# Performance work log

Measured on AMD Instinct MI355X. Metric: run time of the kernel, lower is better.

## Reference

```python
import jax, jax.numpy as jnp
import numpy as np

EPS = 1e-6
BANDWIDTH = 10


def _norm_last(x):
    return x / jnp.sum(x, axis=-1, keepdims=True)


def _causal_linear_branch(Q, K, V, eps):
    # Q,K: [N,L,H,E] feature-mapped; V: [N,L,H,D]
    Q = _norm_last(Q)
    K = _norm_last(K)
    Kcum = jnp.cumsum(K, axis=1)                                   # [N,L,H,E]
    Z = 1.0 / (jnp.einsum('nlhe,nlhe->nlh', Q, Kcum) + eps)        # [N,L,H]
    # causal_dot_product: running sum of outer products K_s V_s^T
    S = jnp.cumsum(K[..., :, None] * V[..., None, :], axis=1)       # [N,L,H,E,D]
    Vn = jnp.einsum('nlhe,nlhed->nlhd', Q, S)                       # [N,L,H,D]
    return Vn * Z[..., None]


def setup_inputs() -> dict:
    key = jax.random.key(0)
    k1, k2, k3, k4 = jax.random.split(key, 4)
    N, L, H, E = 2, 2048, 8, 32
    return {
        'queries': jax.random.normal(k1, (N, L, H, E), dtype=jnp.float32),
        'keys': jax.random.normal(k2, (N, L, H, E), dtype=jnp.float32),
        'values': jax.random.normal(k3, (N, L, H, E), dtype=jnp.float32),
        'key_lengths': jnp.ones((N, L), dtype=jnp.float32),
        'W1': 0.02 * jax.random.normal(k4, (1, 1, H, E), dtype=jnp.float32),
        'W2': jnp.ones((1, 1, H, E), dtype=jnp.float32) * 0.5,
        'W3': jnp.ones((1, 1, H, E), dtype=jnp.float32) * 0.5,
    }


def reference(queries, keys, values, key_lengths, W1, W2, W3):
    klen = key_lengths[:, :, None, None]
    # kernel 1: elu feature map phi(x) = elu(x) + 1
    Q1 = jax.nn.elu(queries) + 1.0
    K1 = (jax.nn.elu(keys) + 1.0) * klen
    LV = W2 * _causal_linear_branch(Q1, K1, values, EPS)
    # kernel 2: squared elu feature map phi(x) = (elu(x) + 1)^2
    Q2 = (jax.nn.elu(queries) + 1.0) ** 2
    K2 = ((jax.nn.elu(keys) + 1.0) ** 2) * klen
    LV = LV + W3 * _causal_linear_branch(Q2, K2, values, EPS)
    # sparse near-field: banded causal softmax attention
    N, L, H, E = queries.shape
    temp = 1.0 / np.sqrt(E).astype(np.float32)
    QK = jnp.einsum('nlhe,nshe->nhls', queries * temp, keys)       # [N,H,L,S]
    li = jnp.arange(L)[:, None]
    si = jnp.arange(L)[None, :]
    band = (si <= li) & (si > li - BANDWIDTH)                      # keep band of width `bandwidth`
    QK = jnp.where(band[None, None], QK, -jnp.inf)
    A = jax.nn.softmax(QK, axis=-1)                                # dropout is identity (p=0 / eval)
    SV = jnp.einsum('nhls,nshd->nlhd', A, values)
    return W1 * SV + LV
```

## Files before the change

### kernel.cpp

```cpp
#include <hip/hip_runtime.h>
#include <cmath>

constexpr int NN = 2;
constexpr int LL = 2048;
constexpr int HH = 8;
constexpr int EE = 32;
constexpr int CC = 32;
constexpr int NCH = LL / CC;
constexpr int NB  = NN * HH * NCH;
constexpr int BWD = 10;
constexpr int REC  = 2 * (EE * EE + EE);
constexpr int R16  = REC * 2 / 16;
constexpr int OFF_S1 = 0, OFF_K1 = 1024, OFF_S2 = 1056, OFF_K2 = 2080;
constexpr int SK = EE + 4;
constexpr int SB = 40;

using f32x16 = __attribute__((ext_vector_type(16))) float;
using s16x8  = __attribute__((ext_vector_type(8)))  short;

__device__ __forceinline__ float elu1(float x) {
    return x > 0.f ? x + 1.f : __expf(x);
}
__device__ __forceinline__ unsigned short bfr(float x) {
    union { float f; unsigned u; } v; v.f = x;
    return (unsigned short)((v.u + 0x7FFFu + ((v.u >> 16) & 1u)) >> 16);
}
__device__ __forceinline__ float bf2f(unsigned short b) {
    union { unsigned u; float f; } v; v.u = ((unsigned)b) << 16;
    return v.f;
}

__global__ __launch_bounds__(256) void chunksum_kernel(
    const float* __restrict__ Kin, const float* __restrict__ Vin,
    unsigned short* __restrict__ ws)
{
    __shared__ float K1n[CC][SK];
    __shared__ float K2n[CC][SK];
    __shared__ float Vs [CC][SK];

    const int b  = blockIdx.x;
    const int c  = b & (NCH - 1);
    const int nh = b >> 6;
    const int t  = threadIdx.x;
    const int lane = t & 31;
    const int grp  = t >> 5;

    for (int r = grp; r < CC; r += 8) {
        const int l = c * CC + r;
        const int base = ((nh >> 3) * LL + l) * HH * EE + (nh & 7) * EE + lane;
        const float k = Kin[base];
        const float v = Vin[base];
        const float f1 = elu1(k);
        const float f2 = f1 * f1;
        float s1 = f1, s2 = f2;
        #pragma unroll
        for (int m = 1; m < 32; m <<= 1) {
            s1 += __shfl_xor(s1, m, 32);
            s2 += __shfl_xor(s2, m, 32);
        }
        K1n[r][lane] = f1 * __builtin_amdgcn_rcpf(s1);
        K2n[r][lane] = f2 * __builtin_amdgcn_rcpf(s2);
        Vs [r][lane] = v;
    }
    __syncthreads();

    const int d  = t >> 3;
    const int e0 = (t & 7) * 4;
    float a1x=0.f,a1y=0.f,a1z=0.f,a1w=0.f;
    float a2x=0.f,a2y=0.f,a2z=0.f,a2w=0.f;
    float k1x=0.f,k1y=0.f,k1z=0.f,k1w=0.f;
    float k2x=0.f,k2y=0.f,k2z=0.f,k2w=0.f;
    for (int j = 0; j < CC; ++j) {
        const float vv = Vs[j][d];
        const float4 k1 = *(const float4*)&K1n[j][e0];
        const float4 k2 = *(const float4*)&K2n[j][e0];
        k1x += k1.x; k1y += k1.y; k1z += k1.z; k1w += k1.w;
        k2x += k2.x; k2y += k2.y; k2z += k2.z; k2w += k2.w;
        a1x += vv * k1.x; a1y += vv * k1.y; a1z += vv * k1.z; a1w += vv * k1.w;
        a2x += vv * k2.x; a2y += vv * k2.y; a2z += vv * k2.z; a2w += vv * k2.w;
    }
    unsigned short* wb = ws + (size_t)b * REC;
    ushort4 o1 = { bfr(a1x), bfr(a1y), bfr(a1z), bfr(a1w) };
    ushort4 o2 = { bfr(a2x), bfr(a2y), bfr(a2z), bfr(a2w) };
    *(ushort4*)&wb[OFF_S1 + d * EE + e0] = o1;
    *(ushort4*)&wb[OFF_S2 + d * EE + e0] = o2;
    if (d == 0) {
        ushort4 s1v = { bfr(k1x), bfr(k1y), bfr(k1z), bfr(k1w) };
        ushort4 s2v = { bfr(k2x), bfr(k2y), bfr(k2z), bfr(k2w) };
        *(ushort4*)&wb[OFF_K1 + e0] = s1v;
        *(ushort4*)&wb[OFF_K2 + e0] = s2v;
    }
}

__global__ __launch_bounds__(192) void prefix_kernel(unsigned short* __restrict__ ws)
{
    const int g = blockIdx.x / 11;
    const int e = (blockIdx.x % 11) * 192 + threadIdx.x;
    unsigned short* base = ws + (size_t)g * NCH * REC + e;
    float run = 0.f;
    {
        unsigned short v[32];
        #pragma unroll
        for (int c = 0; c < 32; ++c) v[c] = base[(size_t)c * REC];
        #pragma unroll
        for (int c = 0; c < 32; ++c) {
            base[(size_t)c * REC] = bfr(run);
            run += bf2f(v[c]);
        }
    }
    {
        unsigned short v[32];
        #pragma unroll
        for (int c = 0; c < 32; ++c) v[c] = base[(size_t)(32 + c) * REC];
        #pragma unroll
        for (int c = 0; c < 32; ++c) {
            base[(size_t)(32 + c) * REC] = bfr(run);
            run += bf2f(v[c]);
        }
    }
}

__global__ __launch_bounds__(256) void fused_kernel(
    const float* __restrict__ Qin, const float* __restrict__ Kin,
    const float* __restrict__ Vin,
    const float* __restrict__ W1, const float* __restrict__ W2,
    const float* __restrict__ W3, const unsigned short* __restrict__ ws,
    float* __restrict__ out)
{
    __shared__ float Vs [CC + 9][SK];
    __shared__ __align__(16) unsigned short Qfb[CC][SB];
    __shared__ __align__(16) unsigned short Kfb[CC][SB];
    __shared__ __align__(16) unsigned short Pb1[CC][SB];
    __shared__ __align__(16) unsigned short Pb2[CC][SB];
    __shared__ float Ob1[CC][SK];
    __shared__ float Ob2[CC][SK];
    __shared__ __align__(16) union {
        float kr[(CC + 9) * SK];
        unsigned short sp[REC];
    } U;

    const int b  = blockIdx.x;
    const int c  = b & (NCH - 1);
    const int nh = b >> 6;
    const int h  = nh & 7;
    const int n  = nh >> 3;
    const int l0 = c * CC;
    const int t  = threadIdx.x;
    const int lane = t & 31;
    const int grp  = t >> 5;

    const uint4* wbv = (const uint4*)(ws + (size_t)b * REC);
    const uint4 s0 = wbv[t];
    uint4 s1 = {0u, 0u, 0u, 0u};
    if (t < R16 - 256) s1 = wbv[256 + t];

    for (int r = grp; r < CC; r += 8) {
        const int l = l0 + r;
        const int base = ((n * LL + l) * HH + h) * EE + lane;
        const float k = Kin[base];
        const float v = Vin[base];
        const float q = Qin[base];
        Kfb[r][lane] = bfr(elu1(k));
        Qfb[r][lane] = bfr(elu1(q));
        Vs[9 + r][lane] = v;
        U.kr[(9 + r) * SK + lane] = k;
    }
    for (int idx = t; idx < 9 * 32; idx += 256) {
        const int rr = idx >> 5, ln = idx & 31;
        const int l = l0 - 9 + rr;
        float kv = 0.f, vv = 0.f;
        if (l >= 0) {
            const int gbase = ((n * LL + l) * HH + h) * EE + ln;
            kv = Kin[gbase];
            vv = Vin[gbase];
        }
        U.kr[rr * SK + ln] = kv;
        Vs[rr][ln] = vv;
    }

    const int r   = t >> 3;
    const int sub = t & 7;
    const int d0  = sub * 4;
    const int l   = l0 + r;

    const float4 q4 = *(const float4*)&Qin[((n * LL + l) * HH + h) * EE + d0];
    __syncthreads();

    float bnd[4];
    {
        const float temp = 0.17677669529663687f;
        float mx = -INFINITY, den = 0.f;
        float sv0 = 0.f, sv1 = 0.f, sv2 = 0.f, sv3 = 0.f;
        #pragma unroll
        for (int jj = 0; jj < BWD; ++jj) {
            const int j = l - (BWD - 1) + jj;
            if (j >= 0) {
                const float4 k4 = *(const float4*)&U.kr[(r + jj) * SK + d0];
                float p = q4.x*k4.x + q4.y*k4.y + q4.z*k4.z + q4.w*k4.w;
                p += __shfl_xor(p, 1, 8); p += __shfl_xor(p, 2, 8); p += __shfl_xor(p, 4, 8);
                const float s  = p * temp;
                const float mn = fmaxf(mx, s);
                const float c1 = __expf(mx - mn);
                const float c2 = __expf(s - mn);
                const float4 v4 = *(const float4*)&Vs[r + jj][d0];
                den = den * c1 + c2;
                sv0 = sv0 * c1 + c2 * v4.x;
                sv1 = sv1 * c1 + c2 * v4.y;
                sv2 = sv2 * c1 + c2 * v4.z;
                sv3 = sv3 * c1 + c2 * v4.w;
                mx = mn;
            }
        }
        const float inv = 1.f / den;
        const float4 w1 = *(const float4*)&W1[h * EE + d0];
        bnd[0] = w1.x * sv0 * inv; bnd[1] = w1.y * sv1 * inv;
        bnd[2] = w1.z * sv2 * inv; bnd[3] = w1.w * sv3 * inv;
    }
    __syncthreads();

    ((uint4*)U.sp)[t] = s0;
    if (t < R16 - 256) ((uint4*)U.sp)[256 + t] = s1;
    __syncthreads();

    const int wid = t >> 6;
    const int l64 = t & 63;
    const int l31 = l64 & 31;
    const int hi5 = l64 >> 5;

    if ((wid & 1) == 0) {
        const bool b2 = (wid == 2);
        const unsigned short* Spt = U.sp + (b2 ? OFF_S2 : OFF_S1);
        const unsigned short* kp  = U.sp + (b2 ? OFF_K2 : OFF_K1);
        const float* Wv = b2 ? W3 : W2;
        unsigned short* Pb = b2 ? &Pb2[0][0] : &Pb1[0][0];
        float* Ob = b2 ? &Ob2[0][0] : &Ob1[0][0];

        s16x8 qa0 = *(const s16x8*)&Qfb[l31][8 * hi5];
        s16x8 qa1 = *(const s16x8*)&Qfb[l31][16 + 8 * hi5];
        s16x8 kb0 = *(const s16x8*)&Kfb[l31][8 * hi5];
        s16x8 kb1 = *(const s16x8*)&Kfb[l31][16 + 8 * hi5];
        if (b2) {
            #pragma unroll
            for (int i = 0; i < 8; ++i) {
                float f;
                f = bf2f((unsigned short)qa0[i]); qa0[i] = (short)bfr(f * f);
                f = bf2f((unsigned short)qa1[i]); qa1[i] = (short)bfr(f * f);
                f = bf2f((unsigned short)kb0[i]); kb0[i] = (short)bfr(f * f);
                f = bf2f((unsigned short)kb1[i]); kb1[i] = (short)bfr(f * f);
            }
        }
        s16x8 ones;
        #pragma unroll
        for (int i = 0; i < 8; ++i) ones[i] = (short)0x3F80;

        f32x16 Dk = {};
        Dk = __builtin_amdgcn_mfma_f32_32x32x16_bf16(ones, kb0, Dk, 0, 0, 0);
        Dk = __builtin_amdgcn_mfma_f32_32x32x16_bf16(ones, kb1, Dk, 0, 0, 0);
        f32x16 P = {};
        P = __builtin_amdgcn_mfma_f32_32x32x16_bf16(qa0, kb0, P, 0, 0, 0);
        P = __builtin_amdgcn_mfma_f32_32x32x16_bf16(qa1, kb1, P, 0, 0, 0);

        const float ki = __builtin_amdgcn_rcpf(Dk[0]);
        #pragma unroll
        for (int k = 0; k < 16; ++k) {
            const int row = (k & 3) + 8 * (k >> 2) + 4 * hi5;
            Pb[row * SB + l31] = bfr((l31 <= row) ? P[k] * ki : 0.f);
        }
        const s16x8 pa0 = *(const s16x8*)&Pb[l31 * SB + 8 * hi5];
        const s16x8 pa1 = *(const s16x8*)&Pb[l31 * SB + 16 + 8 * hi5];

        s16x8 vb0, vb1;
        #pragma unroll
        for (int i = 0; i < 8; ++i) {
            vb0[i] = (short)bfr(Vs[9 + 8 * hi5 + i][l31]);
            vb1[i] = (short)bfr(Vs[9 + 16 + 8 * hi5 + i][l31]);
        }
        const s16x8 sb0 = *(const s16x8*)&Spt[l31 * EE + 8 * hi5];
        const s16x8 sb1 = *(const s16x8*)&Spt[l31 * EE + 16 + 8 * hi5];
        const s16x8 rb0 = *(const s16x8*)&kp[8 * hi5];
        const s16x8 rb1 = *(const s16x8*)&kp[16 + 8 * hi5];

        f32x16 A = {};
        A = __builtin_amdgcn_mfma_f32_32x32x16_bf16(pa0, vb0, A, 0, 0, 0);
        A = __builtin_amdgcn_mfma_f32_32x32x16_bf16(pa1, vb1, A, 0, 0, 0);
        A = __builtin_amdgcn_mfma_f32_32x32x16_bf16(qa0, sb0, A, 0, 0, 0);
        A = __builtin_amdgcn_mfma_f32_32x32x16_bf16(qa1, sb1, A, 0, 0, 0);

        f32x16 Dp = {};
        Dp = __builtin_amdgcn_mfma_f32_32x32x16_bf16(pa0, ones, Dp, 0, 0, 0);
        Dp = __builtin_amdgcn_mfma_f32_32x32x16_bf16(pa1, ones, Dp, 0, 0, 0);
        Dp = __builtin_amdgcn_mfma_f32_32x32x16_bf16(qa0, rb0, Dp, 0, 0, 0);
        Dp = __builtin_amdgcn_mfma_f32_32x32x16_bf16(qa1, rb1, Dp, 0, 0, 0);

        const float wv = Wv[h * EE + l31];
        #pragma unroll
        for (int k = 0; k < 16; ++k) {
            const int row = (k & 3) + 8 * (k >> 2) + 4 * hi5;
            Ob[row * SK + l31] = wv * A[k] * __builtin_amdgcn_rcpf(Dp[k]);
        }
    }
    __syncthreads();

    const float4 o1 = *(const float4*)&Ob1[r][d0];
    const float4 o2 = *(const float4*)&Ob2[r][d0];
    float4 o;
    o.x = bnd[0] + o1.x + o2.x;
    o.y = bnd[1] + o1.y + o2.y;
    o.z = bnd[2] + o1.z + o2.z;
    o.w = bnd[3] + o1.w + o2.w;
    *(float4*)&out[((n * LL + l) * HH + h) * EE + d0] = o;
}

extern "C" void kernel_launch(void* const* d_in, const int* in_sizes, int n_in,
                              void* d_out, int out_size, void* d_ws, size_t ws_size,
                              hipStream_t stream)
{
    (void)in_sizes; (void)n_in; (void)out_size; (void)ws_size;
    const float* Q  = (const float*)d_in[0];
    const float* K  = (const float*)d_in[1];
    const float* V  = (const float*)d_in[2];
    const float* W1 = (const float*)d_in[4];
    const float* W2 = (const float*)d_in[5];
    const float* W3 = (const float*)d_in[6];
    float* out = (float*)d_out;
    unsigned short* ws = (unsigned short*)d_ws;

    chunksum_kernel<<<NB,           256, 0, stream>>>(K, V, ws);
    prefix_kernel  <<<NN * HH * 11, 192, 0, stream>>>(ws);
    fused_kernel   <<<NB,           256, 0, stream>>>(Q, K, V, W1, W2, W3, ws, out);
}
```

Baseline: 101.6 us.

## Fold chunk prefix sum into fused kernel, drop separate prefix launch

Removes the prefix_kernel launch. Each fused block now reads every preceding chunk's bf16 state record from the workspace and sums them in fp32 registers before staging into shared memory. This saves one kernel launch and its serial global round trip. In exchange, total workspace reads grow quadratically in chunk count (up to 63 records for the last chunk), and blocks become load-imbalanced.

```diff
diff --git a/kernel.cpp b/kernel.cpp
--- a/kernel.cpp
+++ b/kernel.cpp
@@ -28,6 +28,12 @@
 __device__ __forceinline__ float bf2f(unsigned short b) {
     union { unsigned u; float f; } v; v.u = ((unsigned)b) << 16;
     return v.f;
+}
+__device__ __forceinline__ float blo(unsigned u) {
+    union { unsigned x; float f; } v; v.x = u << 16; return v.f;
+}
+__device__ __forceinline__ float bhi(unsigned u) {
+    union { unsigned x; float f; } v; v.x = u & 0xffff0000u; return v.f;
 }
 
 __global__ __launch_bounds__(256) void chunksum_kernel(
@@ -92,33 +98,11 @@
     }
 }
 
-__global__ __launch_bounds__(192) void prefix_kernel(unsigned short* __restrict__ ws)
-{
-    const int g = blockIdx.x / 11;
-    const int e = (blockIdx.x % 11) * 192 + threadIdx.x;
-    unsigned short* base = ws + (size_t)g * NCH * REC + e;
-    float run = 0.f;
-    {
-        unsigned short v[32];
-        #pragma unroll
-        for (int c = 0; c < 32; ++c) v[c] = base[(size_t)c * REC];
-        #pragma unroll
-        for (int c = 0; c < 32; ++c) {
-            base[(size_t)c * REC] = bfr(run);
-            run += bf2f(v[c]);
-        }
-    }
-    {
-        unsigned short v[32];
-        #pragma unroll
-        for (int c = 0; c < 32; ++c) v[c] = base[(size_t)(32 + c) * REC];
-        #pragma unroll
-        for (int c = 0; c < 32; ++c) {
-            base[(size_t)(32 + c) * REC] = bfr(run);
-            run += bf2f(v[c]);
-        }
-    }
-}
+#define ACC8(A, V) do { \
+    A[0] += blo((V).x); A[1] += bhi((V).x); \
+    A[2] += blo((V).y); A[3] += bhi((V).y); \
+    A[4] += blo((V).z); A[5] += bhi((V).z); \
+    A[6] += blo((V).w); A[7] += bhi((V).w); } while (0)
 
 __global__ __launch_bounds__(256) void fused_kernel(
     const float* __restrict__ Qin, const float* __restrict__ Kin,
@@ -149,11 +133,6 @@
     const int lane = t & 31;
     const int grp  = t >> 5;
 
-    const uint4* wbv = (const uint4*)(ws + (size_t)b * REC);
-    const uint4 s0 = wbv[t];
-    uint4 s1 = {0u, 0u, 0u, 0u};
-    if (t < R16 - 256) s1 = wbv[256 + t];
-
     for (int r = grp; r < CC; r += 8) {
         const int l = l0 + r;
         const int base = ((n * LL + l) * HH + h) * EE + lane;
@@ -176,6 +155,48 @@
         }
         U.kr[rr * SK + ln] = kv;
         Vs[rr][ln] = vv;
+    }
+
+    float la[8]; float lb[8];
+    #pragma unroll
+    for (int i = 0; i < 8; ++i) { la[i] = 0.f; lb[i] = 0.f; }
+    {
+        const uint4* rb4 = (const uint4*)ws;
+        const size_t p0 = (size_t)(b - c) * R16 + t;
+        const bool tail = (t < 8);
+        int j = 0;
+        for (; j + 8 <= c; j += 8) {
+            uint4 v0 = rb4[p0 + (size_t)(j+0) * R16];
+            uint4 v1 = rb4[p0 + (size_t)(j+1) * R16];
+            uint4 v2 = rb4[p0 + (size_t)(j+2) * R16];
+            uint4 v3 = rb4[p0 + (size_t)(j+3) * R16];
+            uint4 v4 = rb4[p0 + (size_t)(j+4) * R16];
+            uint4 v5 = rb4[p0 + (size_t)(j+5) * R16];
+            uint4 v6 = rb4[p0 + (size_t)(j+6) * R16];
+            uint4 v7 = rb4[p0 + (size_t)(j+7) * R16];
+            if (tail) {
+                uint4 w0 = rb4[p0 + 256 + (size_t)(j+0) * R16];
+                uint4 w1 = rb4[p0 + 256 + (size_t)(j+1) * R16];
+                uint4 w2 = rb4[p0 + 256 + (size_t)(j+2) * R16];
+                uint4 w3 = rb4[p0 + 256 + (size_t)(j+3) * R16];
+                uint4 w4 = rb4[p0 + 256 + (size_t)(j+4) * R16];
+                uint4 w5 = rb4[p0 + 256 + (size_t)(j+5) * R16];
+                uint4 w6 = rb4[p0 + 256 + (size_t)(j+6) * R16];
+                uint4 w7 = rb4[p0 + 256 + (size_t)(j+7) * R16];
+                ACC8(lb, w0); ACC8(lb, w1); ACC8(lb, w2); ACC8(lb, w3);
+                ACC8(lb, w4); ACC8(lb, w5); ACC8(lb, w6); ACC8(lb, w7);
+            }
+            ACC8(la, v0); ACC8(la, v1); ACC8(la, v2); ACC8(la, v3);
+            ACC8(la, v4); ACC8(la, v5); ACC8(la, v6); ACC8(la, v7);
+        }
+        for (; j < c; ++j) {
+            uint4 v = rb4[p0 + (size_t)j * R16];
+            if (tail) {
+                uint4 w = rb4[p0 + 256 + (size_t)j * R16];
+                ACC8(lb, w);
+            }
+            ACC8(la, v);
+        }
     }
 
     const int r   = t >> 3;
@@ -218,8 +239,22 @@
     }
     __syncthreads();
 
-    ((uint4*)U.sp)[t] = s0;
-    if (t < R16 - 256) ((uint4*)U.sp)[256 + t] = s1;
+    {
+        uint4 o;
+        o.x = (unsigned)bfr(la[0]) | ((unsigned)bfr(la[1]) << 16);
+        o.y = (unsigned)bfr(la[2]) | ((unsigned)bfr(la[3]) << 16);
+        o.z = (unsigned)bfr(la[4]) | ((unsigned)bfr(la[5]) << 16);
+        o.w = (unsigned)bfr(la[6]) | ((unsigned)bfr(la[7]) << 16);
+        ((uint4*)U.sp)[t] = o;
+        if (t < 8) {
+            uint4 ob;
+            ob.x = (unsigned)bfr(lb[0]) | ((unsigned)bfr(lb[1]) << 16);
+            ob.y = (unsigned)bfr(lb[2]) | ((unsigned)bfr(lb[3]) << 16);
+            ob.z = (unsigned)bfr(lb[4]) | ((unsigned)bfr(lb[5]) << 16);
+            ob.w = (unsigned)bfr(lb[6]) | ((unsigned)bfr(lb[7]) << 16);
+            ((uint4*)U.sp)[256 + t] = ob;
+        }
+    }
     __syncthreads();
 
     const int wid = t >> 6;
@@ -325,7 +360,6 @@
     float* out = (float*)d_out;
     unsigned short* ws = (unsigned short*)d_ws;
 
-    chunksum_kernel<<<NB,           256, 0, stream>>>(K, V, ws);
-    prefix_kernel  <<<NN * HH * 11, 192, 0, stream>>>(ws);
-    fused_kernel   <<<NB,           256, 0, stream>>>(Q, K, V, W1, W2, W3, ws, out);
-}
+    chunksum_kernel<<<NB, 256, 0, stream>>>(K, V, ws);
+    fused_kernel   <<<NB, 256, 0, stream>>>(Q, K, V, W1, W2, W3, ws, out);
+}
```

New measurement: 114.6 us. +12.9%, slower.

## Compute chunk K^T V sums with bf16 MFMA and pre-transpose V in LDS

Applied to the files above, without the earlier changes.

The chunk-summary kernel now stores normalized K1/K2 and V transposed as bf16 in shared memory and computes the per-chunk outer-product sums and K column sums with 32x32x16 bf16 MFMAs in two waves, replacing the scalar FMA loop. The fused kernel also keeps a bf16 transposed copy of V so the MFMA B operands load as vectors instead of eight scalar reads plus conversions each. The aim is to cut ALU and LDS work in both kernels. In exchange, inputs are rounded to bf16 before accumulation, and only two of the four waves do the matmul.

```diff
diff --git a/kernel.cpp b/kernel.cpp
--- a/kernel.cpp
+++ b/kernel.cpp
@@ -34,9 +34,9 @@
     const float* __restrict__ Kin, const float* __restrict__ Vin,
     unsigned short* __restrict__ ws)
 {
-    __shared__ float K1n[CC][SK];
-    __shared__ float K2n[CC][SK];
-    __shared__ float Vs [CC][SK];
+    __shared__ __align__(16) unsigned short K1T[EE][SB];
+    __shared__ __align__(16) unsigned short K2T[EE][SB];
+    __shared__ __align__(16) unsigned short VT [EE][SB];
 
     const int b  = blockIdx.x;
     const int c  = b & (NCH - 1);
@@ -58,37 +58,42 @@
             s1 += __shfl_xor(s1, m, 32);
             s2 += __shfl_xor(s2, m, 32);
         }
-        K1n[r][lane] = f1 * __builtin_amdgcn_rcpf(s1);
-        K2n[r][lane] = f2 * __builtin_amdgcn_rcpf(s2);
-        Vs [r][lane] = v;
-    }
-    __syncthreads();
-
-    const int d  = t >> 3;
-    const int e0 = (t & 7) * 4;
-    float a1x=0.f,a1y=0.f,a1z=0.f,a1w=0.f;
-    float a2x=0.f,a2y=0.f,a2z=0.f,a2w=0.f;
-    float k1x=0.f,k1y=0.f,k1z=0.f,k1w=0.f;
-    float k2x=0.f,k2y=0.f,k2z=0.f,k2w=0.f;
-    for (int j = 0; j < CC; ++j) {
-        const float vv = Vs[j][d];
-        const float4 k1 = *(const float4*)&K1n[j][e0];
-        const float4 k2 = *(const float4*)&K2n[j][e0];
-        k1x += k1.x; k1y += k1.y; k1z += k1.z; k1w += k1.w;
-        k2x += k2.x; k2y += k2.y; k2z += k2.z; k2w += k2.w;
-        a1x += vv * k1.x; a1y += vv * k1.y; a1z += vv * k1.z; a1w += vv * k1.w;
-        a2x += vv * k2.x; a2y += vv * k2.y; a2z += vv * k2.z; a2w += vv * k2.w;
-    }
-    unsigned short* wb = ws + (size_t)b * REC;
-    ushort4 o1 = { bfr(a1x), bfr(a1y), bfr(a1z), bfr(a1w) };
-    ushort4 o2 = { bfr(a2x), bfr(a2y), bfr(a2z), bfr(a2w) };
-    *(ushort4*)&wb[OFF_S1 + d * EE + e0] = o1;
-    *(ushort4*)&wb[OFF_S2 + d * EE + e0] = o2;
-    if (d == 0) {
-        ushort4 s1v = { bfr(k1x), bfr(k1y), bfr(k1z), bfr(k1w) };
-        ushort4 s2v = { bfr(k2x), bfr(k2y), bfr(k2z), bfr(k2w) };
-        *(ushort4*)&wb[OFF_K1 + e0] = s1v;
-        *(ushort4*)&wb[OFF_K2 + e0] = s2v;
+        K1T[lane][r] = bfr(f1 * __builtin_amdgcn_rcpf(s1));
+        K2T[lane][r] = bfr(f2 * __builtin_amdgcn_rcpf(s2));
+        VT [lane][r] = bfr(v);
+    }
+    __syncthreads();
+
+    const int wid = t >> 6;
+    const int l64 = t & 63;
+    const int l31 = l64 & 31;
+    const int hi5 = l64 >> 5;
+
+    if (wid < 2) {
+        const unsigned short* KT = wid ? &K2T[0][0] : &K1T[0][0];
+        const s16x8 va0 = *(const s16x8*)&VT[l31][8 * hi5];
+        const s16x8 va1 = *(const s16x8*)&VT[l31][16 + 8 * hi5];
+        const s16x8 kb0 = *(const s16x8*)&KT[l31 * SB + 8 * hi5];
+        const s16x8 kb1 = *(const s16x8*)&KT[l31 * SB + 16 + 8 * hi5];
+        s16x8 ones;
+        #pragma unroll
+        for (int i = 0; i < 8; ++i) ones[i] = (short)0x3F80;
+
+        f32x16 S = {};
+        S = __builtin_amdgcn_mfma_f32_32x32x16_bf16(va0, kb0, S, 0, 0, 0);
+        S = __builtin_amdgcn_mfma_f32_32x32x16_bf16(va1, kb1, S, 0, 0, 0);
+        f32x16 Dk = {};
+        Dk = __builtin_amdgcn_mfma_f32_32x32x16_bf16(ones, kb0, Dk, 0, 0, 0);
+        Dk = __builtin_amdgcn_mfma_f32_32x32x16_bf16(ones, kb1, Dk, 0, 0, 0);
+
+        unsigned short* wb = ws + (size_t)b * REC + (wid ? OFF_S2 : OFF_S1);
+        unsigned short* wk = ws + (size_t)b * REC + (wid ? OFF_K2 : OFF_K1);
+        #pragma unroll
+        for (int k = 0; k < 16; ++k) {
+            const int row = (k & 3) + 8 * (k >> 2) + 4 * hi5;
+            wb[row * EE + l31] = bfr(S[k]);
+        }
+        if (hi5 == 0) wk[l31] = bfr(Dk[0]);
     }
 }
 
@@ -130,6 +135,7 @@
     __shared__ float Vs [CC + 9][SK];
     __shared__ __align__(16) unsigned short Qfb[CC][SB];
     __shared__ __align__(16) unsigned short Kfb[CC][SB];
+    __shared__ __align__(16) unsigned short Vtb[EE][SB];
     __shared__ __align__(16) unsigned short Pb1[CC][SB];
     __shared__ __align__(16) unsigned short Pb2[CC][SB];
     __shared__ float Ob1[CC][SK];
@@ -163,6 +169,7 @@
         Kfb[r][lane] = bfr(elu1(k));
         Qfb[r][lane] = bfr(elu1(q));
         Vs[9 + r][lane] = v;
+        Vtb[lane][r] = bfr(v);
         U.kr[(9 + r) * SK + lane] = k;
     }
     for (int idx = t; idx < 9 * 32; idx += 256) {
@@ -269,12 +276,8 @@
         const s16x8 pa0 = *(const s16x8*)&Pb[l31 * SB + 8 * hi5];
         const s16x8 pa1 = *(const s16x8*)&Pb[l31 * SB + 16 + 8 * hi5];
 
-        s16x8 vb0, vb1;
-        #pragma unroll
-        for (int i = 0; i < 8; ++i) {
-            vb0[i] = (short)bfr(Vs[9 + 8 * hi5 + i][l31]);
-            vb1[i] = (short)bfr(Vs[9 + 16 + 8 * hi5 + i][l31]);
-        }
+        const s16x8 vb0 = *(const s16x8*)&Vtb[l31][8 * hi5];
+        const s16x8 vb1 = *(const s16x8*)&Vtb[l31][16 + 8 * hi5];
         const s16x8 sb0 = *(const s16x8*)&Spt[l31 * EE + 8 * hi5];
         const s16x8 sb1 = *(const s16x8*)&Spt[l31 * EE + 16 + 8 * hi5];
         const s16x8 rb0 = *(const s16x8*)&kp[8 * hi5];
```

Result: faster. 90.14 us (-11.3%).
